# Optimization experiments

Measured on AMD Instinct MI355X. Metric: run time of the kernel, lower is better.

## Reference

```python
import math
import jax, jax.numpy as jnp
import numpy as np

B, N, D, H = 8, 128, 256, 8
DK = D // H
SCALE = 0.02


def setup_inputs() -> dict:
    key = jax.random.key(0)
    ks = jax.random.split(key, 10)
    return {
        "query_node": jax.random.normal(ks[0], (B, N, D), jnp.float32),
        "value_node": jax.random.normal(ks[1], (B, N, D), jnp.float32),
        "key_edge": jax.random.normal(ks[2], (B, N, N, D), jnp.float32),
        "adj_matrix": jax.random.uniform(ks[3], (B, N, N), jnp.float32),  # pairwise distances >= 0
        "mask": jnp.ones((B, N), jnp.int32),
        "Wq": jax.random.normal(ks[4], (D, D), jnp.float32) * SCALE,
        "bq": jnp.zeros((D,), jnp.float32),
        "Wk": jax.random.normal(ks[5], (D, D), jnp.float32) * SCALE,
        "bk": jnp.zeros((D,), jnp.float32),
        "Wv": jax.random.normal(ks[6], (D, D), jnp.float32) * SCALE,
        "bv": jnp.zeros((D,), jnp.float32),
        "Wno": jax.random.normal(ks[7], (D, D), jnp.float32) * SCALE,
        "bno": jnp.zeros((D,), jnp.float32),
        "Weo": jax.random.normal(ks[8], (D, D), jnp.float32) * SCALE,
        "beo": jnp.zeros((D,), jnp.float32),
        "att_lambda": jnp.float32(0.1),
    }


def reference(query_node, value_node, key_edge, adj_matrix, mask,
              Wq, bq, Wk, bk, Wv, bv, Wno, bno, Weo, beo, att_lambda):
    # distance-kernelized adjacency: softmax(-lambda * dist) over neighbors
    adj = att_lambda * adj_matrix                                  # [B,N,N]
    adj = jnp.where(mask[:, None, :] == 0, jnp.inf, adj)
    adj = jax.nn.softmax(-adj, axis=-1)                            # [B,N,N]

    q = (query_node @ Wq.T + bq).reshape(B, N, H, DK).transpose(0, 2, 1, 3)      # [B,H,N,DK] bhmd
    k = (key_edge @ Wk.T + bk).reshape(B, N, N, H, DK).transpose(0, 3, 1, 2, 4)  # [B,H,N,N,DK] bhmnd
    v = (value_node @ Wv.T + bv).reshape(B, N, H, DK).transpose(0, 2, 1, 3)      # [B,H,N,DK] bhnd

    inv_sqrt = 1.0 / math.sqrt(DK)
    out_scores = jnp.einsum('bhmd,bhmnd->bhmn', q, k) * inv_sqrt
    in_scores = jnp.einsum('bhnd,bhmnd->bhnm', q, k) * inv_sqrt

    m4 = mask[:, None, None, :] == 0                               # [B,1,1,N]
    neg_inf = jnp.asarray(-jnp.inf, out_scores.dtype)
    out_scores = jnp.where(m4, neg_inf, out_scores)
    in_scores = jnp.where(m4, neg_inf, in_scores)

    out_attn = jax.nn.softmax(out_scores, axis=-1)
    in_attn = jax.nn.softmax(in_scores, axis=-1)

    # message = out_attn + in_attn - diag_embed(diag(out_attn))
    eye = jnp.eye(N, dtype=out_attn.dtype)
    message = out_attn + in_attn - out_attn * eye
    message = message * adj[:, None]                               # adjacency gating (dropout = identity at eval)

    node_hidden = jnp.einsum('bhmn,bhnd->bhmd', message, v)        # [B,H,N,DK]
    edge_hidden = message[..., None] * k                           # [B,H,N,N,DK] outer-product edge update

    node_hidden = node_hidden.transpose(0, 2, 1, 3).reshape(B, N, D)
    edge_hidden = edge_hidden.transpose(0, 2, 3, 1, 4).reshape(B, N, N, D)

    return (node_hidden @ Wno.T + bno, edge_hidden @ Weo.T + beo)
```

## Files before the change

kernel.cpp:

```cpp
#include <hip/hip_runtime.h>
#include <math.h>

#define Bc 8
#define Nc 128
#define Dc 256
#define Hc 8
#define DKc 32

typedef __attribute__((ext_vector_type(8))) short short8;
typedef __attribute__((ext_vector_type(4))) float floatx4;

__device__ __forceinline__ unsigned short f2bf(float f) {
  unsigned int u = __float_as_uint(f);
  u += 0x7FFFu + ((u >> 16) & 1u);
  return (unsigned short)(u >> 16);
}

__global__ __launch_bounds__(256) void cast_bf16_kernel(
    const float* __restrict__ src, unsigned short* __restrict__ dst, int n) {
  const int i = (blockIdx.x * 256 + threadIdx.x) * 4;
  if (i < n) {
    const float4 v = *(const float4*)&src[i];
    *(ushort4*)&dst[i] = make_ushort4(f2bf(v.x), f2bf(v.y), f2bf(v.z), f2bf(v.w));
  }
}

__global__ __launch_bounds__(256) void gemm_xwT_kernel(
    const float* __restrict__ X, const float* __restrict__ W,
    const float* __restrict__ bias, float* __restrict__ C, int M) {
  __shared__ float As[64][17];
  __shared__ float Ws[64][17];
  const int t = threadIdx.x;
  const int tx = t & 15;
  const int ty = t >> 4;
  const size_t row0 = (size_t)blockIdx.y * 64;
  const int col0 = blockIdx.x * 64;
  const int lr = t >> 2;
  const int lc = (t & 3) * 4;

  float acc[4][4] = {};

  for (int kk = 0; kk < 256; kk += 16) {
    float4 av = *(const float4*)&X[(row0 + lr) * 256 + kk + lc];
    float4 wv = *(const float4*)&W[(size_t)(col0 + lr) * 256 + kk + lc];
    As[lr][lc] = av.x; As[lr][lc + 1] = av.y; As[lr][lc + 2] = av.z; As[lr][lc + 3] = av.w;
    Ws[lr][lc] = wv.x; Ws[lr][lc + 1] = wv.y; Ws[lr][lc + 2] = wv.z; Ws[lr][lc + 3] = wv.w;
    __syncthreads();
#pragma unroll
    for (int e = 0; e < 16; ++e) {
      float a[4], w[4];
#pragma unroll
      for (int r = 0; r < 4; ++r) a[r] = As[ty * 4 + r][e];
#pragma unroll
      for (int c = 0; c < 4; ++c) w[c] = Ws[tx * 4 + c][e];
#pragma unroll
      for (int r = 0; r < 4; ++r)
#pragma unroll
        for (int c = 0; c < 4; ++c) acc[r][c] = fmaf(a[r], w[c], acc[r][c]);
    }
    __syncthreads();
  }

  const float4 bv = *(const float4*)&bias[col0 + tx * 4];
#pragma unroll
  for (int r = 0; r < 4; ++r) {
    float4 o;
    o.x = acc[r][0] + bv.x;
    o.y = acc[r][1] + bv.y;
    o.z = acc[r][2] + bv.z;
    o.w = acc[r][3] + bv.w;
    *(float4*)&C[(row0 + ty * 4 + r) * 256 + col0 + tx * 4] = o;
  }
}

__global__ __launch_bounds__(128) void adj_softmax_kernel(
    const float* __restrict__ adj, const int* __restrict__ mask,
    const float* __restrict__ lam_p, float* __restrict__ adjs) {
  __shared__ float red[128];
  const int bi = blockIdx.x;
  const int b = bi >> 7;
  const int j = threadIdx.x;
  const float lam = lam_p[0];
  float x = (mask[b * 128 + j] != 0) ? (-lam * adj[(size_t)bi * 128 + j]) : -INFINITY;
  red[j] = x; __syncthreads();
  for (int s = 64; s > 0; s >>= 1) { if (j < s) red[j] = fmaxf(red[j], red[j + s]); __syncthreads(); }
  const float mx = red[0]; __syncthreads();
  const float e = expf(x - mx);
  red[j] = e; __syncthreads();
  for (int s = 64; s > 0; s >>= 1) { if (j < s) red[j] += red[j + s]; __syncthreads(); }
  const float z = red[0];
  adjs[(size_t)bi * 128 + j] = e / z;
}

__global__ __launch_bounds__(256) void kscore_kernel(
    const float* __restrict__ ke, const float* __restrict__ q,
    const unsigned short* __restrict__ wk, const float* __restrict__ bk,
    float* __restrict__ osc, float* __restrict__ isc) {
  __shared__ __align__(16) unsigned short As[64 * 40];
  __shared__ __align__(16) unsigned short Ws[256 * 40];
  const int nblk = blockIdx.x;
  const int bm = blockIdx.y;
  const int b = bm >> 7;
  const int m = bm & 127;
  const int n0 = nblk * 64;
  const int t = threadIdx.x;
  const int l = t & 63;
  const int w = t >> 6;
  const int lr = l & 15;
  const int lk = l >> 4;
  const size_t rowbase = ((size_t)bm * 128 + n0) * 256;

  floatx4 acc[4][4] = {};

  for (int kk = 0; kk < 256; kk += 32) {
    float4 av[2]; int arow[2], akc[2];
#pragma unroll
    for (int p = 0; p < 2; ++p) {
      const int f = p * 256 + t;
      arow[p] = f >> 3; akc[p] = (f & 7) * 4;
      av[p] = *(const float4*)&ke[rowbase + (size_t)arow[p] * 256 + kk + akc[p]];
    }
    uint4 wv[4];
#pragma unroll
    for (int p = 0; p < 4; ++p) {
      const int f = p * 256 + t;
      const int row = f >> 2, kc = (f & 3) * 8;
      wv[p] = *(const uint4*)&wk[(size_t)row * 256 + kk + kc];
    }
    __syncthreads();
#pragma unroll
    for (int p = 0; p < 2; ++p)
      *(ushort4*)&As[arow[p] * 40 + akc[p]] =
          make_ushort4(f2bf(av[p].x), f2bf(av[p].y), f2bf(av[p].z), f2bf(av[p].w));
#pragma unroll
    for (int p = 0; p < 4; ++p) {
      const int f = p * 256 + t;
      const int row = f >> 2, kc = (f & 3) * 8;
      *(uint4*)&Ws[row * 40 + kc] = wv[p];
    }
    __syncthreads();
    short8 a[4], bw[4];
#pragma unroll
    for (int i = 0; i < 4; ++i)
      a[i] = *(const short8*)&As[(i * 16 + lr) * 40 + lk * 8];
#pragma unroll
    for (int j = 0; j < 4; ++j)
      bw[j] = *(const short8*)&Ws[(w * 64 + j * 16 + lr) * 40 + lk * 8];
#pragma unroll
    for (int i = 0; i < 4; ++i)
#pragma unroll
      for (int j = 0; j < 4; ++j)
        acc[i][j] = __builtin_amdgcn_mfma_f32_16x16x32_bf16(bw[j], a[i], acc[i][j], 0, 0, 0);
  }

  const float inv_sqrt = 0.17677669529663687f;
  float4 qm4[4], kb4[4];
#pragma unroll
  for (int j = 0; j < 4; ++j) {
    qm4[j] = *(const float4*)&q[((size_t)(b * 128 + m)) * 256 + w * 64 + j * 16 + lk * 4];
    kb4[j] = *(const float4*)&bk[w * 64 + j * 16 + lk * 4];
  }
#pragma unroll
  for (int i = 0; i < 4; ++i) {
    const int ng = n0 + i * 16 + lr;
    const size_t qnb = ((size_t)(b * 128 + ng)) * 256 + w * 64 + lk * 4;
    float po0 = 0.f, po1 = 0.f, pi0 = 0.f, pi1 = 0.f;
#pragma unroll
    for (int j = 0; j < 4; ++j) {
      const float4 qn = *(const float4*)&q[qnb + j * 16];
      const float k0 = acc[i][j][0] + kb4[j].x;
      const float k1 = acc[i][j][1] + kb4[j].y;
      const float k2 = acc[i][j][2] + kb4[j].z;
      const float k3 = acc[i][j][3] + kb4[j].w;
      const float so = fmaf(k0, qm4[j].x, fmaf(k1, qm4[j].y, fmaf(k2, qm4[j].z, k3 * qm4[j].w)));
      const float si = fmaf(k0, qn.x, fmaf(k1, qn.y, fmaf(k2, qn.z, k3 * qn.w)));
      if (j < 2) { po0 += so; pi0 += si; } else { po1 += so; pi1 += si; }
    }
    po0 += __shfl_xor(po0, 16, 64); po0 += __shfl_xor(po0, 32, 64);
    po1 += __shfl_xor(po1, 16, 64); po1 += __shfl_xor(po1, 32, 64);
    pi0 += __shfl_xor(pi0, 16, 64); pi0 += __shfl_xor(pi0, 32, 64);
    pi1 += __shfl_xor(pi1, 16, 64); pi1 += __shfl_xor(pi1, 32, 64);
    if (lk == 0) {
      const int h0 = w * 2, h1 = w * 2 + 1;
      osc[((size_t)(b * 8 + h0) * 128 + m) * 128 + ng] = po0 * inv_sqrt;
      osc[((size_t)(b * 8 + h1) * 128 + m) * 128 + ng] = po1 * inv_sqrt;
      isc[((size_t)(b * 8 + h0) * 128 + ng) * 128 + m] = pi0 * inv_sqrt;
      isc[((size_t)(b * 8 + h1) * 128 + ng) * 128 + m] = pi1 * inv_sqrt;
    }
  }
}

__global__ __launch_bounds__(128) void message_kernel(
    const float* __restrict__ osc, const float* __restrict__ isc,
    const float* __restrict__ adjs, const int* __restrict__ mask,
    float* __restrict__ msg) {
  __shared__ float red[128];
  const int bhi = blockIdx.x;
  const int i = bhi & 127;
  const int b = bhi >> 10;
  const int j = threadIdx.x;
  const bool mj = mask[b * 128 + j] != 0;

  const float so = mj ? osc[(size_t)bhi * 128 + j] : -INFINITY;
  const float si = mj ? isc[(size_t)bhi * 128 + j] : -INFINITY;

  red[j] = so; __syncthreads();
  for (int s = 64; s > 0; s >>= 1) { if (j < s) red[j] = fmaxf(red[j], red[j + s]); __syncthreads(); }
  const float mo = red[0]; __syncthreads();
  const float eo = expf(so - mo);
  red[j] = eo; __syncthreads();
  for (int s = 64; s > 0; s >>= 1) { if (j < s) red[j] += red[j + s]; __syncthreads(); }
  const float zo = red[0]; __syncthreads();
  const float oa = eo / zo;

  red[j] = si; __syncthreads();
  for (int s = 64; s > 0; s >>= 1) { if (j < s) red[j] = fmaxf(red[j], red[j + s]); __syncthreads(); }
  const float mi = red[0]; __syncthreads();
  const float ei = expf(si - mi);
  red[j] = ei; __syncthreads();
  for (int s = 64; s > 0; s >>= 1) { if (j < s) red[j] += red[j + s]; __syncthreads(); }
  const float zi = red[0];
  const float ia = ei / zi;

  float val = oa + ia - ((i == j) ? oa : 0.0f);
  val *= adjs[((size_t)(b * 128 + i)) * 128 + j];
  msg[(size_t)bhi * 128 + j] = val;
}

__global__ __launch_bounds__(256) void node_hidden_kernel(
    const float* __restrict__ msg, const float* __restrict__ v,
    float* __restrict__ nh) {
  __shared__ float Ms[32][129];
  __shared__ float Vs[128][33];
  const int blk = blockIdx.x;
  const int mblk = blk & 3;
  const int bh = blk >> 2;
  const int h = bh & 7;
  const int b = bh >> 3;
  const int t = threadIdx.x;

  {
    const int n = t & 127, r0 = t >> 7;
#pragma unroll
    for (int p = 0; p < 16; ++p) {
      const int r = r0 + p * 2;
      Ms[r][n] = msg[((size_t)bh * 128 + mblk * 32 + r) * 128 + n];
    }
  }
  {
    const int dk = t & 31, n0 = t >> 5;
#pragma unroll
    for (int p = 0; p < 16; ++p) {
      const int n = n0 + p * 8;
      Vs[n][dk] = v[((size_t)b * 128 + n) * 256 + h * 32 + dk];
    }
  }
  __syncthreads();

  const int dk = t & 31;
  const int mg = t >> 5;
  float acc[4] = {0.f, 0.f, 0.f, 0.f};
  for (int n = 0; n < 128; ++n) {
    const float vv = Vs[n][dk];
#pragma unroll
    for (int r = 0; r < 4; ++r) acc[r] = fmaf(Ms[mg + 8 * r][n], vv, acc[r]);
  }
#pragma unroll
  for (int r = 0; r < 4; ++r) {
    const int m = mblk * 32 + mg + 8 * r;
    nh[((size_t)b * 128 + m) * 256 + h * 32 + dk] = acc[r];
  }
}

__global__ __launch_bounds__(256) void edge_fused_kernel(
    const float* __restrict__ ke, const float* __restrict__ msg,
    const unsigned short* __restrict__ wk, const unsigned short* __restrict__ weo,
    const float* __restrict__ bk, const float* __restrict__ beo,
    float* __restrict__ out) {
  __shared__ __align__(16) unsigned short As[64 * 40];
  __shared__ __align__(16) unsigned short Ws[256 * 40];
  __shared__ __align__(16) unsigned short K1[64 * 264];
  __shared__ float Msgs[64][8];
  const int nblk = blockIdx.x;
  const int bm = blockIdx.y;
  const int b = bm >> 7;
  const int m = bm & 127;
  const int n0 = nblk * 64;
  const int t = threadIdx.x;
  const int l = t & 63;
  const int w = t >> 6;
  const int lr = l & 15;
  const int lk = l >> 4;
  const size_t rowbase = ((size_t)bm * 128 + n0) * 256;

#pragma unroll
  for (int p = 0; p < 2; ++p) {
    const int idx = t + p * 256;
    const int r = idx >> 3, h = idx & 7;
    Msgs[r][h] = msg[(((size_t)(b * 8 + h) * 128 + m) * 128) + n0 + r];
  }

  floatx4 acc[4][4] = {};

  for (int kk = 0; kk < 256; kk += 32) {
    float4 av[2]; int arow[2], akc[2];
#pragma unroll
    for (int p = 0; p < 2; ++p) {
      const int f = p * 256 + t;
      arow[p] = f >> 3; akc[p] = (f & 7) * 4;
      av[p] = *(const float4*)&ke[rowbase + (size_t)arow[p] * 256 + kk + akc[p]];
    }
    uint4 wv[4];
#pragma unroll
    for (int p = 0; p < 4; ++p) {
      const int f = p * 256 + t;
      const int row = f >> 2, kc = (f & 3) * 8;
      wv[p] = *(const uint4*)&wk[(size_t)row * 256 + kk + kc];
    }
    __syncthreads();
#pragma unroll
    for (int p = 0; p < 2; ++p)
      *(ushort4*)&As[arow[p] * 40 + akc[p]] =
          make_ushort4(f2bf(av[p].x), f2bf(av[p].y), f2bf(av[p].z), f2bf(av[p].w));
#pragma unroll
    for (int p = 0; p < 4; ++p) {
      const int f = p * 256 + t;
      const int row = f >> 2, kc = (f & 3) * 8;
      *(uint4*)&Ws[row * 40 + kc] = wv[p];
    }
    __syncthreads();
    short8 a[4], bw[4];
#pragma unroll
    for (int i = 0; i < 4; ++i)
      a[i] = *(const short8*)&As[(i * 16 + lr) * 40 + lk * 8];
#pragma unroll
    for (int j = 0; j < 4; ++j)
      bw[j] = *(const short8*)&Ws[(w * 64 + j * 16 + lr) * 40 + lk * 8];
#pragma unroll
    for (int i = 0; i < 4; ++i)
#pragma unroll
      for (int j = 0; j < 4; ++j)
        acc[i][j] = __builtin_amdgcn_mfma_f32_16x16x32_bf16(bw[j], a[i], acc[i][j], 0, 0, 0);
  }

#pragma unroll
  for (int j = 0; j < 4; ++j) {
    const int col = w * 64 + j * 16 + lk * 4;
    const float4 kb = *(const float4*)&bk[col];
    const int h = col >> 5;
#pragma unroll
    for (int i = 0; i < 4; ++i) {
      const int row = i * 16 + lr;
      const float sc = Msgs[row][h];
      *(ushort4*)&K1[row * 264 + col] = make_ushort4(
          f2bf((acc[i][j][0] + kb.x) * sc), f2bf((acc[i][j][1] + kb.y) * sc),
          f2bf((acc[i][j][2] + kb.z) * sc), f2bf((acc[i][j][3] + kb.w) * sc));
      acc[i][j] = (floatx4){0.f, 0.f, 0.f, 0.f};
    }
  }
  __syncthreads();

  for (int kk = 0; kk < 256; kk += 32) {
    uint4 wv[4];
#pragma unroll
    for (int p = 0; p < 4; ++p) {
      const int f = p * 256 + t;
      const int row = f >> 2, kc = (f & 3) * 8;
      wv[p] = *(const uint4*)&weo[(size_t)row * 256 + kk + kc];
    }
    __syncthreads();
#pragma unroll
    for (int p = 0; p < 4; ++p) {
      const int f = p * 256 + t;
      const int row = f >> 2, kc = (f & 3) * 8;
      *(uint4*)&Ws[row * 40 + kc] = wv[p];
    }
    __syncthreads();
    short8 ak[4], bw[4];
#pragma unroll
    for (int i = 0; i < 4; ++i)
      ak[i] = *(const short8*)&K1[(i * 16 + lr) * 264 + kk + lk * 8];
#pragma unroll
    for (int j = 0; j < 4; ++j)
      bw[j] = *(const short8*)&Ws[(w * 64 + j * 16 + lr) * 40 + lk * 8];
#pragma unroll
    for (int i = 0; i < 4; ++i)
#pragma unroll
      for (int j = 0; j < 4; ++j)
        acc[i][j] = __builtin_amdgcn_mfma_f32_16x16x32_bf16(bw[j], ak[i], acc[i][j], 0, 0, 0);
  }

  float4 bj[4];
#pragma unroll
  for (int j = 0; j < 4; ++j) bj[j] = *(const float4*)&beo[w * 64 + j * 16 + lk * 4];
#pragma unroll
  for (int i = 0; i < 4; ++i) {
    const size_t rb = rowbase + (size_t)(i * 16 + lr) * 256;
#pragma unroll
    for (int j = 0; j < 4; ++j) {
      float4 o;
      o.x = acc[i][j][0] + bj[j].x;
      o.y = acc[i][j][1] + bj[j].y;
      o.z = acc[i][j][2] + bj[j].z;
      o.w = acc[i][j][3] + bj[j].w;
      *(float4*)&out[rb + w * 64 + j * 16 + lk * 4] = o;
    }
  }
}

extern "C" void kernel_launch(void* const* d_in, const int* in_sizes, int n_in,
                              void* d_out, int out_size, void* d_ws, size_t ws_size,
                              hipStream_t stream) {
  (void)in_sizes; (void)n_in; (void)out_size; (void)ws_size;
  const float* query_node = (const float*)d_in[0];
  const float* value_node = (const float*)d_in[1];
  const float* key_edge   = (const float*)d_in[2];
  const float* adj_matrix = (const float*)d_in[3];
  const int*   mask       = (const int*)d_in[4];
  const float* Wq  = (const float*)d_in[5];
  const float* bq  = (const float*)d_in[6];
  const float* Wk  = (const float*)d_in[7];
  const float* bk  = (const float*)d_in[8];
  const float* Wv  = (const float*)d_in[9];
  const float* bv  = (const float*)d_in[10];
  const float* Wno = (const float*)d_in[11];
  const float* bno = (const float*)d_in[12];
  const float* Weo = (const float*)d_in[13];
  const float* beo = (const float*)d_in[14];
  const float* lam = (const float*)d_in[15];

  float* out = (float*)d_out;
  float* node_out = out;
  float* edge_out = out + (size_t)Bc * Nc * Dc;

  float* ws = (float*)d_ws;
  float* q    = ws; ws += (size_t)Bc * Nc * Dc;
  float* v    = ws; ws += (size_t)Bc * Nc * Dc;
  float* adjs = ws; ws += (size_t)Bc * Nc * Nc;
  float* osc  = ws; ws += (size_t)Bc * Hc * Nc * Nc;
  float* isc  = ws; ws += (size_t)Bc * Hc * Nc * Nc;
  float* msg  = ws; ws += (size_t)Bc * Hc * Nc * Nc;
  float* nh   = ws; ws += (size_t)Bc * Nc * Dc;
  unsigned short* wkbf  = (unsigned short*)ws; ws += 32768;
  unsigned short* weobf = (unsigned short*)ws; ws += 32768;

  cast_bf16_kernel<<<dim3(64), 256, 0, stream>>>(Wk, wkbf, Dc * Dc);
  cast_bf16_kernel<<<dim3(64), 256, 0, stream>>>(Weo, weobf, Dc * Dc);
  gemm_xwT_kernel<<<dim3(4, 16), 256, 0, stream>>>(query_node, Wq, bq, q, Bc * Nc);
  gemm_xwT_kernel<<<dim3(4, 16), 256, 0, stream>>>(value_node, Wv, bv, v, Bc * Nc);
  adj_softmax_kernel<<<dim3(Bc * Nc), 128, 0, stream>>>(adj_matrix, mask, lam, adjs);
  kscore_kernel<<<dim3(2, 1024), 256, 0, stream>>>(key_edge, q, wkbf, bk, osc, isc);
  message_kernel<<<dim3(Bc * Hc * Nc), 128, 0, stream>>>(osc, isc, adjs, mask, msg);
  node_hidden_kernel<<<dim3(Bc * Hc * 4), 256, 0, stream>>>(msg, v, nh);
  gemm_xwT_kernel<<<dim3(4, 16), 256, 0, stream>>>(nh, Wno, bno, node_out, Bc * Nc);
  edge_fused_kernel<<<dim3(2, 1024), 256, 0, stream>>>(
      key_edge, msg, wkbf, weobf, bk, beo, edge_out);
}
```

Baseline: 579.5 us.

## Cache projected K as bf16 in the output buffer to skip recomputing it

Measured after the change: 543.2 us. 1.07x faster.

```diff
diff --git a/kernel.cpp b/kernel.cpp
--- a/kernel.cpp
+++ b/kernel.cpp
@@ -14,6 +14,10 @@
   unsigned int u = __float_as_uint(f);
   u += 0x7FFFu + ((u >> 16) & 1u);
   return (unsigned short)(u >> 16);
+}
+
+__device__ __forceinline__ float bf2f(unsigned short s) {
+  return __uint_as_float(((unsigned int)s) << 16);
 }
 
 __global__ __launch_bounds__(256) void cast_bf16_kernel(
@@ -95,7 +99,8 @@
 __global__ __launch_bounds__(256) void kscore_kernel(
     const float* __restrict__ ke, const float* __restrict__ q,
     const unsigned short* __restrict__ wk, const float* __restrict__ bk,
-    float* __restrict__ osc, float* __restrict__ isc) {
+    float* __restrict__ osc, float* __restrict__ isc,
+    float* __restrict__ edge ) {
   __shared__ __align__(16) unsigned short As[64 * 40];
   __shared__ __align__(16) unsigned short Ws[256 * 40];
   const int nblk = blockIdx.x;
@@ -109,6 +114,7 @@
   const int lr = l & 15;
   const int lk = l >> 4;
   const size_t rowbase = ((size_t)bm * 128 + n0) * 256;
+  unsigned short* kbf = (unsigned short*)edge;
 
   floatx4 acc[4][4] = {};
 
@@ -163,6 +169,7 @@
 #pragma unroll
   for (int i = 0; i < 4; ++i) {
     const int ng = n0 + i * 16 + lr;
+    const size_t gkb = (size_t)bm * 128 + ng;
     const size_t qnb = ((size_t)(b * 128 + ng)) * 256 + w * 64 + lk * 4;
     float po0 = 0.f, po1 = 0.f, pi0 = 0.f, pi1 = 0.f;
 #pragma unroll
@@ -172,6 +179,8 @@
       const float k1 = acc[i][j][1] + kb4[j].y;
       const float k2 = acc[i][j][2] + kb4[j].z;
       const float k3 = acc[i][j][3] + kb4[j].w;
+      *(ushort4*)&kbf[gkb * 512 + 256 + w * 64 + j * 16 + lk * 4] =
+          make_ushort4(f2bf(k0), f2bf(k1), f2bf(k2), f2bf(k3));
       const float so = fmaf(k0, qm4[j].x, fmaf(k1, qm4[j].y, fmaf(k2, qm4[j].z, k3 * qm4[j].w)));
       const float si = fmaf(k0, qn.x, fmaf(k1, qn.y, fmaf(k2, qn.z, k3 * qn.w)));
       if (j < 2) { po0 += so; pi0 += si; } else { po1 += so; pi1 += si; }
@@ -272,14 +281,11 @@
   }
 }
 
-__global__ __launch_bounds__(256) void edge_fused_kernel(
-    const float* __restrict__ ke, const float* __restrict__ msg,
-    const unsigned short* __restrict__ wk, const unsigned short* __restrict__ weo,
-    const float* __restrict__ bk, const float* __restrict__ beo,
-    float* __restrict__ out) {
+__global__ __launch_bounds__(256) void edge2_kernel(
+    float* edge, const float* __restrict__ msg,
+    const unsigned short* __restrict__ weo, const float* __restrict__ beo) {
   __shared__ __align__(16) unsigned short As[64 * 40];
   __shared__ __align__(16) unsigned short Ws[256 * 40];
-  __shared__ __align__(16) unsigned short K1[64 * 264];
   __shared__ float Msgs[64][8];
   const int nblk = blockIdx.x;
   const int bm = blockIdx.y;
@@ -291,7 +297,8 @@
   const int w = t >> 6;
   const int lr = l & 15;
   const int lk = l >> 4;
-  const size_t rowbase = ((size_t)bm * 128 + n0) * 256;
+  const unsigned short* kbf = (const unsigned short*)edge;
+  const size_t g0 = (size_t)bm * 128 + n0;
 
 #pragma unroll
   for (int p = 0; p < 2; ++p) {
@@ -301,27 +308,28 @@
   }
 
   floatx4 acc[4][4] = {};
+  const int arow = t >> 2, akc = (t & 3) * 8;
 
   for (int kk = 0; kk < 256; kk += 32) {
-    float4 av[2]; int arow[2], akc[2];
-#pragma unroll
-    for (int p = 0; p < 2; ++p) {
-      const int f = p * 256 + t;
-      arow[p] = f >> 3; akc[p] = (f & 7) * 4;
-      av[p] = *(const float4*)&ke[rowbase + (size_t)arow[p] * 256 + kk + akc[p]];
-    }
+    const int h = kk >> 5;
+    const uint4 kv = *(const uint4*)&kbf[(g0 + arow) * 512 + 256 + kk + akc];
     uint4 wv[4];
 #pragma unroll
     for (int p = 0; p < 4; ++p) {
       const int f = p * 256 + t;
       const int row = f >> 2, kc = (f & 3) * 8;
-      wv[p] = *(const uint4*)&wk[(size_t)row * 256 + kk + kc];
-    }
-    __syncthreads();
-#pragma unroll
-    for (int p = 0; p < 2; ++p)
-      *(ushort4*)&As[arow[p] * 40 + akc[p]] =
-          make_ushort4(f2bf(av[p].x), f2bf(av[p].y), f2bf(av[p].z), f2bf(av[p].w));
+      wv[p] = *(const uint4*)&weo[(size_t)row * 256 + kk + kc];
+    }
+    __syncthreads();
+    {
+      const float sc = Msgs[arow][h];
+      const unsigned short* us = (const unsigned short*)&kv;
+      unsigned short o[8];
+#pragma unroll
+      for (int e = 0; e < 8; ++e) o[e] = f2bf(bf2f(us[e]) * sc);
+      *(ushort4*)&As[arow * 40 + akc]     = make_ushort4(o[0], o[1], o[2], o[3]);
+      *(ushort4*)&As[arow * 40 + akc + 4] = make_ushort4(o[4], o[5], o[6], o[7]);
+    }
 #pragma unroll
     for (int p = 0; p < 4; ++p) {
       const int f = p * 256 + t;
@@ -343,56 +351,10 @@
         acc[i][j] = __builtin_amdgcn_mfma_f32_16x16x32_bf16(bw[j], a[i], acc[i][j], 0, 0, 0);
   }
 
-#pragma unroll
-  for (int j = 0; j < 4; ++j) {
-    const int col = w * 64 + j * 16 + lk * 4;
-    const float4 kb = *(const float4*)&bk[col];
-    const int h = col >> 5;
-#pragma unroll
-    for (int i = 0; i < 4; ++i) {
-      const int row = i * 16 + lr;
-      const float sc = Msgs[row][h];
-      *(ushort4*)&K1[row * 264 + col] = make_ushort4(
-          f2bf((acc[i][j][0] + kb.x) * sc), f2bf((acc[i][j][1] + kb.y) * sc),
-          f2bf((acc[i][j][2] + kb.z) * sc), f2bf((acc[i][j][3] + kb.w) * sc));
-      acc[i][j] = (floatx4){0.f, 0.f, 0.f, 0.f};
-    }
-  }
-  __syncthreads();
-
-  for (int kk = 0; kk < 256; kk += 32) {
-    uint4 wv[4];
-#pragma unroll
-    for (int p = 0; p < 4; ++p) {
-      const int f = p * 256 + t;
-      const int row = f >> 2, kc = (f & 3) * 8;
-      wv[p] = *(const uint4*)&weo[(size_t)row * 256 + kk + kc];
-    }
-    __syncthreads();
-#pragma unroll
-    for (int p = 0; p < 4; ++p) {
-      const int f = p * 256 + t;
-      const int row = f >> 2, kc = (f & 3) * 8;
-      *(uint4*)&Ws[row * 40 + kc] = wv[p];
-    }
-    __syncthreads();
-    short8 ak[4], bw[4];
-#pragma unroll
-    for (int i = 0; i < 4; ++i)
-      ak[i] = *(const short8*)&K1[(i * 16 + lr) * 264 + kk + lk * 8];
-#pragma unroll
-    for (int j = 0; j < 4; ++j)
-      bw[j] = *(const short8*)&Ws[(w * 64 + j * 16 + lr) * 40 + lk * 8];
-#pragma unroll
-    for (int i = 0; i < 4; ++i)
-#pragma unroll
-      for (int j = 0; j < 4; ++j)
-        acc[i][j] = __builtin_amdgcn_mfma_f32_16x16x32_bf16(bw[j], ak[i], acc[i][j], 0, 0, 0);
-  }
-
   float4 bj[4];
 #pragma unroll
   for (int j = 0; j < 4; ++j) bj[j] = *(const float4*)&beo[w * 64 + j * 16 + lk * 4];
+  const size_t rowbase = g0 * 256;
 #pragma unroll
   for (int i = 0; i < 4; ++i) {
     const size_t rb = rowbase + (size_t)(i * 16 + lr) * 256;
@@ -403,7 +365,7 @@
       o.y = acc[i][j][1] + bj[j].y;
       o.z = acc[i][j][2] + bj[j].z;
       o.w = acc[i][j][3] + bj[j].w;
-      *(float4*)&out[rb + w * 64 + j * 16 + lk * 4] = o;
+      *(float4*)&edge[rb + w * 64 + j * 16 + lk * 4] = o;
     }
   }
 }
@@ -449,10 +411,9 @@
   gemm_xwT_kernel<<<dim3(4, 16), 256, 0, stream>>>(query_node, Wq, bq, q, Bc * Nc);
   gemm_xwT_kernel<<<dim3(4, 16), 256, 0, stream>>>(value_node, Wv, bv, v, Bc * Nc);
   adj_softmax_kernel<<<dim3(Bc * Nc), 128, 0, stream>>>(adj_matrix, mask, lam, adjs);
-  kscore_kernel<<<dim3(2, 1024), 256, 0, stream>>>(key_edge, q, wkbf, bk, osc, isc);
+  kscore_kernel<<<dim3(2, 1024), 256, 0, stream>>>(key_edge, q, wkbf, bk, osc, isc, edge_out);
   message_kernel<<<dim3(Bc * Hc * Nc), 128, 0, stream>>>(osc, isc, adjs, mask, msg);
   node_hidden_kernel<<<dim3(Bc * Hc * 4), 256, 0, stream>>>(msg, v, nh);
   gemm_xwT_kernel<<<dim3(4, 16), 256, 0, stream>>>(nh, Wno, bno, node_out, Bc * Nc);
-  edge_fused_kernel<<<dim3(2, 1024), 256, 0, stream>>>(
-      key_edge, msg, wkbf, weobf, bk, beo, edge_out);
-}
+  edge2_kernel<<<dim3(2, 1024), 256, 0, stream>>>(edge_out, msg, weobf, beo);
+}
```
